# Performance work log

Measured on AMD Instinct MI355X. Metric: run time of the kernel, lower is better.

## Reference

```python
import jax, jax.numpy as jnp
import numpy as np

K = 16

def _knn_idx(pts, k):
    # pts: [B, 3, N] -> idx [B, N, k] (self-inclusive nearest neighbors)
    inner = -2.0 * jnp.einsum('bdn,bdm->bnm', pts, pts)
    xx = jnp.sum(pts * pts, axis=1)  # [B, N]
    pd = -xx[:, :, None] - inner - xx[:, None, :]  # negative squared distance
    _, idx = jax.lax.top_k(pd, k)
    return idx

def _gather(feats, idx):
    # feats: [B, N, D], idx: [B, N, k] -> [B, N, k, D]
    return jax.vmap(lambda f, i: f[i])(feats, idx)

def _conv1x1(x, w, b):
    # x: [B, Cin, N], w: [Cout, Cin], b: [Cout]
    return jnp.einsum('oi,bin->bon', w, x) + b[None, :, None]

def _linear(x, w, b):
    # x: [B, N, Din], w: [Dout, Din]
    return jnp.einsum('bnd,od->bno', x, w) + b

def _local_cov(pts, idx):
    # pts: [B, 3, N] -> [B, 12, N]
    nb = _gather(jnp.swapaxes(pts, 1, 2), idx)  # [B, N, k, 3]
    outer = nb[:, :, 0, :, None] * nb[:, :, 1, None, :]  # [B, N, 3, 3]
    B, N = pts.shape[0], pts.shape[2]
    outer = jnp.swapaxes(outer.reshape(B, N, 9), 1, 2)  # [B, 9, N]
    return jnp.concatenate([pts, outer], axis=1)

def _local_maxpool(x, idx):
    # x: [B, D, N] -> [B, N, D]
    nb = _gather(jnp.swapaxes(x, 1, 2), idx)  # [B, N, k, D]
    return jnp.max(nb, axis=2)

def setup_inputs() -> dict:
    key = jax.random.key(0)
    ks = jax.random.split(key, 20)
    def w(k, shape):
        return jax.random.normal(k, shape, dtype=jnp.float32) * 0.05
    pts = jax.random.normal(ks[0], (8, 3, 4096), dtype=jnp.float32)
    return {
        'pts': pts,
        'm1w1': w(ks[1], (64, 12)), 'm1b1': w(ks[2], (64,)),
        'm1w2': w(ks[3], (64, 64)), 'm1b2': w(ks[4], (64,)),
        'm1w3': w(ks[5], (64, 64)), 'm1b3': w(ks[6], (64,)),
        'l1w': w(ks[7], (64, 64)), 'l1b': w(ks[8], (64,)),
        'c1w': w(ks[9], (128, 64)), 'c1b': w(ks[10], (128,)),
        'l2w': w(ks[11], (128, 128)), 'l2b': w(ks[12], (128,)),
        'c2w': w(ks[13], (1024, 128)), 'c2b': w(ks[14], (1024,)),
        'm2w1': w(ks[15], (512, 1024)), 'm2b1': w(ks[16], (512,)),
        'm2w2': w(ks[17], (512, 512)), 'm2b2': w(ks[18], (512,)),
    }

def reference(pts, m1w1, m1b1, m1w2, m1b2, m1w3, m1b3, l1w, l1b,
              c1w, c1b, l2w, l2b, c2w, c2b, m2w1, m2b1, m2w2, m2b2):
    idx = _knn_idx(pts, K)  # [B, N, k]
    x = _local_cov(pts, idx)  # [B, 12, N]
    # mlp1: three 1x1 convs with ReLU
    x = jax.nn.relu(_conv1x1(x, m1w1, m1b1))
    x = jax.nn.relu(_conv1x1(x, m1w2, m1b2))
    x = jax.nn.relu(_conv1x1(x, m1w3, m1b3))  # [B, 64, N]
    # graph layer
    x = _local_maxpool(x, idx)          # [B, N, 64]
    x = _linear(x, l1w, l1b)            # [B, N, 64]
    x = jnp.swapaxes(x, 1, 2)           # [B, 64, N]
    x = jax.nn.relu(_conv1x1(x, c1w, c1b))  # [B, 128, N]
    x = _local_maxpool(x, idx)          # [B, N, 128]
    x = _linear(x, l2w, l2b)            # [B, N, 128]
    x = jnp.swapaxes(x, 1, 2)           # [B, 128, N]
    x = _conv1x1(x, c2w, c2b)           # [B, 1024, N]
    # global max pool
    x = jnp.max(x, axis=2, keepdims=True)  # [B, 1024, 1]
    # mlp2
    x = jax.nn.relu(_conv1x1(x, m2w1, m2b1))
    x = _conv1x1(x, m2w2, m2b2)  # [B, 512, 1]
    return x.reshape(-1, 512)
```

## Files before the change

### kernel.cpp

```cpp
#include <hip/hip_runtime.h>
#include <cfloat>

#define NBATCH 8
#define NPTS   4096
#define KNN    16
#define PPB    32
#define NSL    8
#define CAP    24

typedef unsigned short u16;
typedef unsigned int   u32;
typedef __attribute__((ext_vector_type(8))) short short8;
typedef __attribute__((ext_vector_type(4))) float f32x4;

__device__ __forceinline__ float relu_f(float x) { return x > 0.f ? x : 0.f; }

__device__ __forceinline__ u32 bf16_split_pack(float v)
{
    unsigned u = __float_as_uint(v);
    unsigned hb = (u + 0x7FFFu + ((u >> 16) & 1u)) >> 16;
    float hf = __uint_as_float(hb << 16);
    float l = v - hf;
    unsigned ul = __float_as_uint(l);
    unsigned lb = (ul + 0x7FFFu + ((ul >> 16) & 1u)) >> 16;
    return (hb << 16) | (lb & 0xFFFFu);
}

__device__ __forceinline__ void unpack8(uint4 a, uint4 b, short8& h, short8& l)
{
    union { unsigned u[4]; short8 s; } H, L;
    H.u[0] = __builtin_amdgcn_perm(a.y, a.x, 0x07060302);
    H.u[1] = __builtin_amdgcn_perm(a.w, a.z, 0x07060302);
    H.u[2] = __builtin_amdgcn_perm(b.y, b.x, 0x07060302);
    H.u[3] = __builtin_amdgcn_perm(b.w, b.z, 0x07060302);
    L.u[0] = __builtin_amdgcn_perm(a.y, a.x, 0x05040100);
    L.u[1] = __builtin_amdgcn_perm(a.w, a.z, 0x05040100);
    L.u[2] = __builtin_amdgcn_perm(b.y, b.x, 0x05040100);
    L.u[3] = __builtin_amdgcn_perm(b.w, b.z, 0x05040100);
    h = H.s; l = L.s;
}

__global__ __launch_bounds__(256)
void knn_kernel(const float* __restrict__ pts, int* __restrict__ idxout)
{
    __shared__ __align__(16) float4 tile[NSL * 129];
    __shared__ float  kl[PPB * NSL * 8];
    __shared__ float  thr[PPB];
    __shared__ int    cnt[PPB];

    const int b = blockIdx.y, tid = threadIdx.x;
    const int ptl = tid >> 3, r = tid & 7;
    const int n = blockIdx.x * PPB + ptl;
    const float* pb = pts + (size_t)b * 3 * NPTS;

    const float sx = pb[n], sy = pb[NPTS + n], sz = pb[2 * NPTS + n];

    float k8[8];
#pragma unroll
    for (int s = 0; s < 8; ++s) k8[s] = -FLT_MAX;

    const float4* slice = tile + r * 129;

    for (int t = 0; t < 4; ++t) {
        if (t) __syncthreads();
        for (int i = tid; i < 1024; i += 256) {
            int j = t * 1024 + i;
            float x = pb[j], y = pb[NPTS + j], z = pb[2 * NPTS + j];
            float xx = __fadd_rn(__fadd_rn(__fmul_rn(x, x), __fmul_rn(y, y)),
                                 __fmul_rn(z, z));
            tile[(i >> 7) * 129 + (i & 127)] = make_float4(x, y, z, xx);
        }
        __syncthreads();
#pragma unroll 8
        for (int ii = 0; ii < 128; ++ii) {
            float4 c = slice[ii];
            float dt = __fmaf_rn(sx, c.x, __fmaf_rn(sy, c.y, __fmul_rn(sz, c.z)));
            float pd = __fmaf_rn(2.f, dt, -c.w);
            float old0 = k8[0];
#pragma unroll
            for (int s = 7; s >= 1; --s)
                k8[s] = __builtin_amdgcn_fmed3f(k8[s - 1], k8[s], pd);
            k8[0] = fmaxf(old0, pd);
        }
    }

#pragma unroll
    for (int s = 0; s < 8; ++s) kl[(ptl * NSL + r) * 8 + s] = k8[s];
    __syncthreads();

    if (r == 0) {
        const float* L = kl + ptl * 64;
        int p0 = 0, p1 = 0, p2 = 0, p3 = 0, p4 = 0, p5 = 0, p6 = 0, p7 = 0;
        float tv = 0.f;
        for (int o = 0; o < 16; ++o) {
            float v0 = (p0 < 8) ? L[p0]      : -FLT_MAX;
            float v1 = (p1 < 8) ? L[8 + p1]  : -FLT_MAX;
            float v2 = (p2 < 8) ? L[16 + p2] : -FLT_MAX;
            float v3 = (p3 < 8) ? L[24 + p3] : -FLT_MAX;
            float v4 = (p4 < 8) ? L[32 + p4] : -FLT_MAX;
            float v5 = (p5 < 8) ? L[40 + p5] : -FLT_MAX;
            float v6 = (p6 < 8) ? L[48 + p6] : -FLT_MAX;
            float v7 = (p7 < 8) ? L[56 + p7] : -FLT_MAX;
            float m = fmaxf(fmaxf(fmaxf(v0, v1), fmaxf(v2, v3)),
                            fmaxf(fmaxf(v4, v5), fmaxf(v6, v7)));
            tv = m;
            if      (v0 == m) ++p0;
            else if (v1 == m) ++p1;
            else if (v2 == m) ++p2;
            else if (v3 == m) ++p3;
            else if (v4 == m) ++p4;
            else if (v5 == m) ++p5;
            else if (v6 == m) ++p6;
            else              ++p7;
        }
        thr[ptl] = tv;
        cnt[ptl] = 0;
    }
    __syncthreads();
    const float myThr = thr[ptl];

    float* pv = kl;
    int*   pi = (int*)(kl + PPB * CAP);

    for (int tt = 0; tt < 4; ++tt) {
        int t = 3 - tt;
        if (tt) {
            __syncthreads();
            for (int i = tid; i < 1024; i += 256) {
                int j = t * 1024 + i;
                float x = pb[j], y = pb[NPTS + j], z = pb[2 * NPTS + j];
                float xx = __fadd_rn(__fadd_rn(__fmul_rn(x, x), __fmul_rn(y, y)),
                                     __fmul_rn(z, z));
                tile[(i >> 7) * 129 + (i & 127)] = make_float4(x, y, z, xx);
            }
            __syncthreads();
        }
#pragma unroll 8
        for (int ii = 0; ii < 128; ++ii) {
            float4 c = slice[ii];
            float dt = __fmaf_rn(sx, c.x, __fmaf_rn(sy, c.y, __fmul_rn(sz, c.z)));
            float pd = __fmaf_rn(2.f, dt, -c.w);
            if (pd >= myThr) {
                int pos = atomicAdd(&cnt[ptl], 1);
                if (pos < CAP) {
                    pv[ptl * CAP + pos] = pd;
                    pi[ptl * CAP + pos] = t * 1024 + r * 128 + ii;
                }
            }
        }
    }
    __syncthreads();

    if (tid < PPB) {
        const int np = blockIdx.x * PPB + tid;
        int* out = idxout + ((size_t)b * NPTS + np) * KNN;
        int c = cnt[tid];
        if (c <= CAP) {
            float* v  = pv + tid * CAP;
            int*   ix = pi + tid * CAP;
            for (int o = 0; o < 16; ++o) {
                int best = o;
                for (int q = o + 1; q < c; ++q) {
                    float vq = v[q], vb = v[best];
                    if (vq > vb || (vq == vb && ix[q] < ix[best])) best = q;
                }
                float tv = v[o]; v[o] = v[best]; v[best] = tv;
                int   ti = ix[o]; ix[o] = ix[best]; ix[best] = ti;
                out[o] = ix[o];
            }
        } else {
            float qx = pb[np], qy = pb[NPTS + np], qz = pb[2 * NPTS + np];
            float v16[16]; int i16[16];
#pragma unroll
            for (int s = 0; s < 16; ++s) { v16[s] = -FLT_MAX; i16[s] = 0; }
            for (int j = 0; j < NPTS; ++j) {
                float x = pb[j], y = pb[NPTS + j], z = pb[2 * NPTS + j];
                float xx = __fadd_rn(__fadd_rn(__fmul_rn(x, x), __fmul_rn(y, y)),
                                     __fmul_rn(z, z));
                float dt = __fmaf_rn(qx, x, __fmaf_rn(qy, y, __fmul_rn(qz, z)));
                float pd = __fmaf_rn(2.f, dt, -xx);
                if (pd > v16[15]) {
                    int s = 15;
                    while (s > 0 && pd > v16[s - 1]) {
                        v16[s] = v16[s - 1]; i16[s] = i16[s - 1]; --s;
                    }
                    v16[s] = pd; i16[s] = j;
                }
            }
            for (int o = 0; o < 16; ++o) out[o] = i16[o];
        }
    }
}

__global__ __launch_bounds__(256)
void cov_mlp1_kernel(const float* __restrict__ pts, const int* __restrict__ idx,
                     const float* __restrict__ w1, const float* __restrict__ b1,
                     const float* __restrict__ w2, const float* __restrict__ b2,
                     const float* __restrict__ w3, const float* __restrict__ b3,
                     float* __restrict__ h3out)
{
    __shared__ __align__(16) float cov[64 * 16];
    __shared__ __align__(16) float w1s[64 * 16];
    __shared__ __align__(16) float w2s[64 * 68];
    __shared__ __align__(16) float w3s[64 * 68];
    __shared__ __align__(16) float hA[64 * 68];
    __shared__ __align__(16) float hB[64 * 68];

    const int b = blockIdx.y, tid = threadIdx.x;
    const int n0 = blockIdx.x * 64;
    const int pq = tid >> 4, cq = tid & 15;

    for (int i = tid; i < 64 * 4; i += 256) {
        int p = i >> 2, k4 = i & 3;
        float4 v = make_float4(0.f, 0.f, 0.f, 0.f);
        if (k4 < 3) v = *(const float4*)(w1 + p * 12 + k4 * 4);
        ((float4*)(w1s + p * 16))[k4] = v;
    }
    for (int i = tid; i < 64 * 16; i += 256) {
        int p = i >> 4, k4 = i & 15;
        ((float4*)(w2s + p * 68))[k4] = ((const float4*)(w2 + p * 64))[k4];
        ((float4*)(w3s + p * 68))[k4] = ((const float4*)(w3 + p * 64))[k4];
    }
    if (tid < 64) {
        const int n = n0 + tid;
        const int* ip = idx + ((size_t)b * NPTS + n) * KNN;
        int j0 = ip[0], j1 = ip[1];
        const float* pb = pts + (size_t)b * 3 * NPTS;
        float px = pb[n],  py = pb[NPTS + n],  pz = pb[2 * NPTS + n];
        float ax = pb[j0], ay = pb[NPTS + j0], az = pb[2 * NPTS + j0];
        float bx = pb[j1], by = pb[NPTS + j1], bz = pb[2 * NPTS + j1];
        float* cv = cov + tid * 16;
        cv[0] = px; cv[1] = py; cv[2] = pz;
        cv[3] = ax * bx; cv[4]  = ax * by; cv[5]  = ax * bz;
        cv[6] = ay * bx; cv[7]  = ay * by; cv[8]  = ay * bz;
        cv[9] = az * bx; cv[10] = az * by; cv[11] = az * bz;
        cv[12] = 0.f; cv[13] = 0.f; cv[14] = 0.f; cv[15] = 0.f;
    }
    __syncthreads();

    {
        float acc[4][4];
#pragma unroll
        for (int i = 0; i < 4; ++i)
#pragma unroll
            for (int j = 0; j < 4; ++j) acc[i][j] = 0.f;
        const float4* X4 = (const float4*)cov;
        const float4* W4 = (const float4*)w1s;
#pragma unroll
        for (int k4 = 0; k4 < 4; ++k4) {
            float4 xa[4], wb[4];
#pragma unroll
            for (int i = 0; i < 4; ++i) xa[i] = X4[(pq * 4 + i) * 4 + k4];
#pragma unroll
            for (int j = 0; j < 4; ++j) wb[j] = W4[(cq + 16 * j) * 4 + k4];
#pragma unroll
            for (int i = 0; i < 4; ++i)
#pragma unroll
                for (int j = 0; j < 4; ++j)
                    acc[i][j] += xa[i].x * wb[j].x + xa[i].y * wb[j].y
                               + xa[i].z * wb[j].z + xa[i].w * wb[j].w;
        }
#pragma unroll
        for (int j = 0; j < 4; ++j) {
            int c = cq + 16 * j;
            float bias = b1[c];
#pragma unroll
            for (int i = 0; i < 4; ++i)
                hA[(pq * 4 + i) * 68 + c] = relu_f(acc[i][j] + bias);
        }
    }
    __syncthreads();

    {
        float acc[4][4];
#pragma unroll
        for (int i = 0; i < 4; ++i)
#pragma unroll
            for (int j = 0; j < 4; ++j) acc[i][j] = 0.f;
        const float4* X4 = (const float4*)hA;
        const float4* W4 = (const float4*)w2s;
        for (int k4 = 0; k4 < 16; ++k4) {
            float4 xa[4], wb[4];
#pragma unroll
            for (int i = 0; i < 4; ++i) xa[i] = X4[(pq * 4 + i) * 17 + k4];
#pragma unroll
            for (int j = 0; j < 4; ++j) wb[j] = W4[(cq + 16 * j) * 17 + k4];
#pragma unroll
            for (int i = 0; i < 4; ++i)
#pragma unroll
                for (int j = 0; j < 4; ++j)
                    acc[i][j] += xa[i].x * wb[j].x + xa[i].y * wb[j].y
                               + xa[i].z * wb[j].z + xa[i].w * wb[j].w;
        }
#pragma unroll
        for (int j = 0; j < 4; ++j) {
            int c = cq + 16 * j;
            float bias = b2[c];
#pragma unroll
            for (int i = 0; i < 4; ++i)
                hB[(pq * 4 + i) * 68 + c] = relu_f(acc[i][j] + bias);
        }
    }
    __syncthreads();

    {
        float acc[4][4];
#pragma unroll
        for (int i = 0; i < 4; ++i)
#pragma unroll
            for (int j = 0; j < 4; ++j) acc[i][j] = 0.f;
        const float4* X4 = (const float4*)hB;
        const float4* W4 = (const float4*)w3s;
        for (int k4 = 0; k4 < 16; ++k4) {
            float4 xa[4], wb[4];
#pragma unroll
            for (int i = 0; i < 4; ++i) xa[i] = X4[(pq * 4 + i) * 17 + k4];
#pragma unroll
            for (int j = 0; j < 4; ++j) wb[j] = W4[(cq + 16 * j) * 17 + k4];
#pragma unroll
            for (int i = 0; i < 4; ++i)
#pragma unroll
                for (int j = 0; j < 4; ++j)
                    acc[i][j] += xa[i].x * wb[j].x + xa[i].y * wb[j].y
                               + xa[i].z * wb[j].z + xa[i].w * wb[j].w;
        }
#pragma unroll
        for (int j = 0; j < 4; ++j) {
            int c = cq + 16 * j;
            float bias = b3[c];
#pragma unroll
            for (int i = 0; i < 4; ++i)
                h3out[((size_t)b * NPTS + n0 + pq * 4 + i) * 64 + c] =
                    relu_f(acc[i][j] + bias);
        }
    }
}

template <int DV4>
__global__ __launch_bounds__(256)
void maxpool4_kernel(const float4* __restrict__ f, const int* __restrict__ idx,
                     float4* __restrict__ out)
{
    constexpr int SH = (DV4 == 16) ? 4 : 5;
    int t = blockIdx.x * 256 + threadIdx.x;
    int d4 = t & (DV4 - 1);
    int n  = (t >> SH) & (NPTS - 1);
    int b  = t >> (SH + 12);
    const int* ip = idx + ((size_t)b * NPTS + n) * KNN;
    const float4* fb = f + (size_t)b * NPTS * DV4;
    float4 v = make_float4(-FLT_MAX, -FLT_MAX, -FLT_MAX, -FLT_MAX);
#pragma unroll
    for (int k = 0; k < KNN; ++k) {
        float4 c = fb[(size_t)ip[k] * DV4 + d4];
        v.x = fmaxf(v.x, c.x); v.y = fmaxf(v.y, c.y);
        v.z = fmaxf(v.z, c.z); v.w = fmaxf(v.w, c.w);
    }
    out[t] = v;
}

__global__ __launch_bounds__(256)
void lin_conv1_kernel(const float* __restrict__ xin,
                      const float* __restrict__ l1w, const float* __restrict__ l1b,
                      const float* __restrict__ c1w, const float* __restrict__ c1b,
                      float* __restrict__ yout)
{
    __shared__ __align__(16) float sx[64 * 68];
    __shared__ __align__(16) float wbuf[64 * 68];
    __shared__ __align__(16) float t1[64 * 68];
    const int b = blockIdx.y, tid = threadIdx.x;
    const int n0 = blockIdx.x * 64;
    const int pq = tid >> 4, cq = tid & 15;

    for (int i = tid; i < 64 * 16; i += 256) {
        int p = i >> 4, k4 = i & 15;
        ((float4*)(sx + p * 68))[k4] =
            ((const float4*)(xin + ((size_t)b * NPTS + n0 + p) * 64))[k4];
        ((float4*)(wbuf + p * 68))[k4] = ((const float4*)(l1w + p * 64))[k4];
    }
    __syncthreads();

    {
        float acc[4][4];
#pragma unroll
        for (int i = 0; i < 4; ++i)
#pragma unroll
            for (int j = 0; j < 4; ++j) acc[i][j] = 0.f;
        const float4* X4 = (const float4*)sx;
        const float4* W4 = (const float4*)wbuf;
        for (int k4 = 0; k4 < 16; ++k4) {
            float4 xa[4], wb[4];
#pragma unroll
            for (int i = 0; i < 4; ++i) xa[i] = X4[(pq * 4 + i) * 17 + k4];
#pragma unroll
            for (int j = 0; j < 4; ++j) wb[j] = W4[(cq + 16 * j) * 17 + k4];
#pragma unroll
            for (int i = 0; i < 4; ++i)
#pragma unroll
                for (int j = 0; j < 4; ++j)
                    acc[i][j] += xa[i].x * wb[j].x + xa[i].y * wb[j].y
                               + xa[i].z * wb[j].z + xa[i].w * wb[j].w;
        }
#pragma unroll
        for (int j = 0; j < 4; ++j) {
            int c = cq + 16 * j;
            float bias = l1b[c];
#pragma unroll
            for (int i = 0; i < 4; ++i)
                t1[(pq * 4 + i) * 68 + c] = acc[i][j] + bias;
        }
    }

    for (int g = 0; g < 2; ++g) {
        __syncthreads();
        for (int i = tid; i < 64 * 16; i += 256) {
            int p = i >> 4, k4 = i & 15;
            ((float4*)(wbuf + p * 68))[k4] =
                ((const float4*)(c1w + (size_t)(g * 64 + p) * 64))[k4];
        }
        __syncthreads();
        float acc[4][4];
#pragma unroll
        for (int i = 0; i < 4; ++i)
#pragma unroll
            for (int j = 0; j < 4; ++j) acc[i][j] = 0.f;
        const float4* X4 = (const float4*)t1;
        const float4* W4 = (const float4*)wbuf;
        for (int k4 = 0; k4 < 16; ++k4) {
            float4 xa[4], wb[4];
#pragma unroll
            for (int i = 0; i < 4; ++i) xa[i] = X4[(pq * 4 + i) * 17 + k4];
#pragma unroll
            for (int j = 0; j < 4; ++j) wb[j] = W4[(cq + 16 * j) * 17 + k4];
#pragma unroll
            for (int i = 0; i < 4; ++i)
#pragma unroll
                for (int j = 0; j < 4; ++j)
                    acc[i][j] += xa[i].x * wb[j].x + xa[i].y * wb[j].y
                               + xa[i].z * wb[j].z + xa[i].w * wb[j].w;
        }
#pragma unroll
        for (int j = 0; j < 4; ++j) {
            int c = g * 64 + cq + 16 * j;
            float bias = c1b[c];
#pragma unroll
            for (int i = 0; i < 4; ++i)
                yout[((size_t)b * NPTS + n0 + pq * 4 + i) * 128 + c] =
                    relu_f(acc[i][j] + bias);
        }
    }
}

__global__ __launch_bounds__(256)
void lin2_kernel(const float* __restrict__ xin, const float* __restrict__ w,
                 const float* __restrict__ bias, u32* __restrict__ xpk)
{
    __shared__ __align__(16) float Xs[64 * 132];
    __shared__ __align__(16) float Ws[64 * 132];
    const int chunk = blockIdx.x, g = blockIdx.y, b = blockIdx.z;
    const int tid = threadIdx.x;

    for (int i = tid; i < 64 * 32; i += 256) {
        int p = i >> 5, k4 = i & 31;
        ((float4*)(Xs + p * 132))[k4] =
            ((const float4*)(xin + ((size_t)b * NPTS + chunk * 64 + p) * 128))[k4];
        ((float4*)(Ws + p * 132))[k4] =
            ((const float4*)(w + (size_t)(g * 64 + p) * 128))[k4];
    }
    __syncthreads();

    const int pq = tid >> 4, cq = tid & 15;
    const float4* X4 = (const float4*)Xs;
    const float4* W4 = (const float4*)Ws;
    float acc[4][4];
#pragma unroll
    for (int i = 0; i < 4; ++i)
#pragma unroll
        for (int j = 0; j < 4; ++j) acc[i][j] = 0.f;

    for (int k4 = 0; k4 < 32; ++k4) {
        float4 xa[4], wb[4];
#pragma unroll
        for (int i = 0; i < 4; ++i) xa[i] = X4[(pq * 4 + i) * 33 + k4];
#pragma unroll
        for (int j = 0; j < 4; ++j) wb[j] = W4[(cq + 16 * j) * 33 + k4];
#pragma unroll
        for (int i = 0; i < 4; ++i)
#pragma unroll
            for (int j = 0; j < 4; ++j)
                acc[i][j] += xa[i].x * wb[j].x + xa[i].y * wb[j].y
                           + xa[i].z * wb[j].z + xa[i].w * wb[j].w;
    }
#pragma unroll
    for (int j = 0; j < 4; ++j) {
        int c = g * 64 + cq + 16 * j;
        float bv = bias[c];
#pragma unroll
        for (int i = 0; i < 4; ++i) {
            float v = acc[i][j] + bv;
            size_t oidx = ((size_t)b * NPTS + chunk * 64 + pq * 4 + i) * 128 + c;
            xpk[oidx] = bf16_split_pack(v);
        }
    }
}

__global__ __launch_bounds__(256)
void wsplit_kernel(const float* __restrict__ w, u32* __restrict__ wpk)
{
    int t = blockIdx.x * 256 + threadIdx.x;
    wpk[t] = bf16_split_pack(w[t]);
}

__global__ __launch_bounds__(256)
void conv2max_mfma(const u32* __restrict__ xpk, const u32* __restrict__ wpk,
                   const float* __restrict__ bias, float* __restrict__ pmax)
{
    __shared__ __align__(16) u16 lds[4 * 16384];
    u16* Wh = lds;
    u16* Wl = lds + 16384;
    u16* Xh = lds + 2 * 16384;
    u16* Xl = lds + 3 * 16384;

    const int chunk = blockIdx.x, g = blockIdx.y, b = blockIdx.z;
    const int tid = threadIdx.x;
    const int lane = tid & 63, wave = tid >> 6;
    const int l15 = lane & 15, l4 = lane >> 4;
    const int wm = wave >> 1, wn = wave & 1;

    const u32* wp_g = wpk + (size_t)g * 128 * 128;
    const u32* xp_g = xpk + ((size_t)b * NPTS + chunk * 128) * 128;

    for (int u = tid; u < 2048; u += 256) {
        int row = u & 127, seg = u >> 7;
        int go = row * 128 + seg * 8;
        int lo_ = seg * 1024 + row * 8;
        uint4 a = *(const uint4*)&wp_g[go];
        uint4 b4 = *(const uint4*)&wp_g[go + 4];
        short8 h, l;
        unpack8(a, b4, h, l);
        *(short8*)&Wh[lo_] = h; *(short8*)&Wl[lo_] = l;
        a = *(const uint4*)&xp_g[go];
        b4 = *(const uint4*)&xp_g[go + 4];
        unpack8(a, b4, h, l);
        *(short8*)&Xh[lo_] = h; *(short8*)&Xl[lo_] = l;
    }
    __syncthreads();

    f32x4 acc[4][4];
#pragma unroll
    for (int mt = 0; mt < 4; ++mt)
#pragma unroll
        for (int nt = 0; nt < 4; ++nt)
            acc[mt][nt] = (f32x4){0.f, 0.f, 0.f, 0.f};

    for (int kb = 0; kb < 4; ++kb) {
        const int seg = kb * 4 + l4;
        short8 Ah[4], Al[4], Bh[4], Bl[4];
#pragma unroll
        for (int mt = 0; mt < 4; ++mt) {
            int off = seg * 1024 + (wm * 64 + mt * 16 + l15) * 8;
            Ah[mt] = *(const short8*)&Wh[off];
            Al[mt] = *(const short8*)&Wl[off];
        }
#pragma unroll
        for (int nt = 0; nt < 4; ++nt) {
            int off = seg * 1024 + (wn * 64 + nt * 16 + l15) * 8;
            Bh[nt] = *(const short8*)&Xh[off];
            Bl[nt] = *(const short8*)&Xl[off];
        }
#pragma unroll
        for (int mt = 0; mt < 4; ++mt)
#pragma unroll
            for (int nt = 0; nt < 4; ++nt) {
                acc[mt][nt] = __builtin_amdgcn_mfma_f32_16x16x32_bf16(
                    Ah[mt], Bh[nt], acc[mt][nt], 0, 0, 0);
                acc[mt][nt] = __builtin_amdgcn_mfma_f32_16x16x32_bf16(
                    Ah[mt], Bl[nt], acc[mt][nt], 0, 0, 0);
                acc[mt][nt] = __builtin_amdgcn_mfma_f32_16x16x32_bf16(
                    Al[mt], Bh[nt], acc[mt][nt], 0, 0, 0);
            }
    }

    __syncthreads();
    float* smax = (float*)lds;
#pragma unroll
    for (int mt = 0; mt < 4; ++mt)
#pragma unroll
        for (int r = 0; r < 4; ++r) {
            float m = fmaxf(fmaxf(acc[mt][0][r], acc[mt][1][r]),
                            fmaxf(acc[mt][2][r], acc[mt][3][r]));
            int c = wm * 64 + mt * 16 + 4 * l4 + r;
            smax[c * 33 + wn * 16 + l15] = m;
        }
    __syncthreads();
    if (tid < 128) {
        const float* row = smax + tid * 33;
        float v = row[0];
#pragma unroll
        for (int j = 1; j < 32; ++j) v = fmaxf(v, row[j]);
        int c = g * 128 + tid;
        pmax[((size_t)b * 32 + chunk) * 1024 + c] = v + bias[c];
    }
}

__global__ __launch_bounds__(256)
void gmax_kernel(const float* __restrict__ pmax, float* __restrict__ gmax)
{
    int t = blockIdx.x * 256 + threadIdx.x;
    int b = t >> 10, ch = t & 1023;
    const float* pp = pmax + (size_t)b * 32 * 1024 + ch;
    float v = -FLT_MAX;
    for (int c = 0; c < 32; ++c) v = fmaxf(v, pp[c * 1024]);
    gmax[t] = v;
}

__global__ __launch_bounds__(128)
void mlp2a_kernel(const float* __restrict__ g, const float* __restrict__ w1,
                  const float* __restrict__ b1, float* __restrict__ h)
{
    __shared__ __align__(16) float sg[1024];
    const int b = blockIdx.y, tid = threadIdx.x;
    for (int i = tid; i < 1024; i += 128) sg[i] = g[b * 1024 + i];
    __syncthreads();
    const int ch = blockIdx.x * 128 + tid;
    const float4* xr = (const float4*)sg;
    const float4* wr = (const float4*)(w1 + (size_t)ch * 1024);
    float a0 = 0.f, a1 = 0.f, a2 = 0.f, a3 = 0.f;
    for (int k = 0; k < 256; ++k) {
        float4 w = wr[k], x = xr[k];
        a0 += w.x * x.x; a1 += w.y * x.y; a2 += w.z * x.z; a3 += w.w * x.w;
    }
    h[b * 512 + ch] = relu_f(b1[ch] + ((a0 + a1) + (a2 + a3)));
}

__global__ __launch_bounds__(128)
void mlp2b_kernel(const float* __restrict__ h, const float* __restrict__ w2,
                  const float* __restrict__ b2, float* __restrict__ out)
{
    __shared__ __align__(16) float sh[512];
    const int b = blockIdx.y, tid = threadIdx.x;
    for (int i = tid; i < 512; i += 128) sh[i] = h[b * 512 + i];
    __syncthreads();
    const int ch = blockIdx.x * 128 + tid;
    const float4* xr = (const float4*)sh;
    const float4* wr = (const float4*)(w2 + (size_t)ch * 512);
    float a0 = 0.f, a1 = 0.f, a2 = 0.f, a3 = 0.f;
    for (int k = 0; k < 128; ++k) {
        float4 w = wr[k], x = xr[k];
        a0 += w.x * x.x; a1 += w.y * x.y; a2 += w.z * x.z; a3 += w.w * x.w;
    }
    out[b * 512 + ch] = b2[ch] + ((a0 + a1) + (a2 + a3));
}

extern "C" void kernel_launch(void* const* d_in, const int* in_sizes, int n_in,
                              void* d_out, int out_size, void* d_ws, size_t ws_size,
                              hipStream_t stream)
{
    const float* pts  = (const float*)d_in[0];
    const float* m1w1 = (const float*)d_in[1];
    const float* m1b1 = (const float*)d_in[2];
    const float* m1w2 = (const float*)d_in[3];
    const float* m1b2 = (const float*)d_in[4];
    const float* m1w3 = (const float*)d_in[5];
    const float* m1b3 = (const float*)d_in[6];
    const float* l1w  = (const float*)d_in[7];
    const float* l1b  = (const float*)d_in[8];
    const float* c1w  = (const float*)d_in[9];
    const float* c1b  = (const float*)d_in[10];
    const float* l2w  = (const float*)d_in[11];
    const float* l2b  = (const float*)d_in[12];
    const float* c2w  = (const float*)d_in[13];
    const float* c2b  = (const float*)d_in[14];
    const float* m2w1 = (const float*)d_in[15];
    const float* m2b1 = (const float*)d_in[16];
    const float* m2w2 = (const float*)d_in[17];
    const float* m2b2 = (const float*)d_in[18];

    char* ws = (char*)d_ws;
    size_t off = 0;
    int*   idx   = (int*)(ws + off);   off += (size_t)NBATCH * NPTS * KNN * 4;
    float* h3    = (float*)(ws + off); off += (size_t)NBATCH * NPTS * 64 * 4;
    float* mp1   = (float*)(ws + off); off += (size_t)NBATCH * NPTS * 64 * 4;
    float* y1    = (float*)(ws + off); off += (size_t)NBATCH * NPTS * 128 * 4;
    float* mp2   = (float*)(ws + off); off += (size_t)NBATCH * NPTS * 128 * 4;
    float* pmaxb = (float*)(ws + off); off += (size_t)NBATCH * 64 * 1024 * 4;
    float* gmx   = (float*)(ws + off); off += (size_t)NBATCH * 1024 * 4;
    float* hbuf  = (float*)(ws + off); off += (size_t)NBATCH * 512 * 4;
    u32*   wpk   = (u32*)(ws + off);   off += (size_t)1024 * 128 * 4;
    u32*   xpk   = (u32*)y1;

    wsplit_kernel<<<dim3(512), 256, 0, stream>>>(c2w, wpk);
    knn_kernel<<<dim3(NPTS / PPB, NBATCH), 256, 0, stream>>>(pts, idx);
    cov_mlp1_kernel<<<dim3(64, NBATCH), 256, 0, stream>>>(pts, idx, m1w1, m1b1,
                                                          m1w2, m1b2, m1w3, m1b3, h3);
    maxpool4_kernel<16><<<dim3(NBATCH * NPTS * 16 / 256), 256, 0, stream>>>(
        (const float4*)h3, idx, (float4*)mp1);
    lin_conv1_kernel<<<dim3(64, NBATCH), 256, 0, stream>>>(mp1, l1w, l1b, c1w, c1b, y1);
    maxpool4_kernel<32><<<dim3(NBATCH * NPTS * 32 / 256), 256, 0, stream>>>(
        (const float4*)y1, idx, (float4*)mp2);
    lin2_kernel<<<dim3(64, 2, NBATCH), 256, 0, stream>>>(mp2, l2w, l2b, xpk);
    conv2max_mfma<<<dim3(32, 8, NBATCH), 256, 0, stream>>>(xpk, wpk, c2b, pmaxb);
    gmax_kernel<<<dim3(32), 256, 0, stream>>>(pmaxb, gmx);
    mlp2a_kernel<<<dim3(4, NBATCH), 128, 0, stream>>>(gmx, m2w1, m2b1, hbuf);
    mlp2b_kernel<<<dim3(4, NBATCH), 128, 0, stream>>>(hbuf, m2w2, m2b2, (float*)d_out);
}
```

Baseline: 299.0 us.

## Split KNN candidate range in halves with two queries per thread, then merge

The KNN kernel now handles 64 query points per block. Each thread keeps two top-8 lists, for queries A and B, so every shared-memory tile load is reused across two queries. Each block scans only half of the candidate points, giving a grid of 64x2x8 blocks, and writes a partial top-16 of values and indices into the y1 scratch buffer. A new merge kernel combines the two sorted halves into the final indices. This adds an extra launch and global traffic for the partial results, plus higher register pressure from the doubled top-k state.

```diff
diff --git a/kernel.cpp b/kernel.cpp
--- a/kernel.cpp
+++ b/kernel.cpp
@@ -4,9 +4,8 @@
 #define NBATCH 8
 #define NPTS   4096
 #define KNN    16
-#define PPB    32
-#define NSL    8
 #define CAP    24
+#define JH     2048
 
 typedef unsigned short u16;
 typedef unsigned int   u32;
@@ -41,55 +40,67 @@
 }
 
 __global__ __launch_bounds__(256)
-void knn_kernel(const float* __restrict__ pts, int* __restrict__ idxout)
-{
-    __shared__ __align__(16) float4 tile[NSL * 129];
-    __shared__ float  kl[PPB * NSL * 8];
-    __shared__ float  thr[PPB];
-    __shared__ int    cnt[PPB];
-
-    const int b = blockIdx.y, tid = threadIdx.x;
+void knn_half_kernel(const float* __restrict__ pts,
+                     float* __restrict__ ppd, int* __restrict__ pix)
+{
+    __shared__ __align__(16) float4 tile[8 * 65];
+    __shared__ float kl[64 * 64];
+    __shared__ float thr[64];
+    __shared__ int   cnt[64];
+
+    const int b = blockIdx.z, half = blockIdx.y, tid = threadIdx.x;
     const int ptl = tid >> 3, r = tid & 7;
-    const int n = blockIdx.x * PPB + ptl;
+    const int n0 = blockIdx.x * 64;
+    const int nA = n0 + ptl, nB = n0 + 32 + ptl;
     const float* pb = pts + (size_t)b * 3 * NPTS;
-
-    const float sx = pb[n], sy = pb[NPTS + n], sz = pb[2 * NPTS + n];
-
-    float k8[8];
-#pragma unroll
-    for (int s = 0; s < 8; ++s) k8[s] = -FLT_MAX;
-
-    const float4* slice = tile + r * 129;
+    const int jb0 = half * JH;
+
+    const float axp = pb[nA], ayp = pb[NPTS + nA], azp = pb[2 * NPTS + nA];
+    const float bxp = pb[nB], byp = pb[NPTS + nB], bzp = pb[2 * NPTS + nB];
+
+    float kA[8], kB[8];
+#pragma unroll
+    for (int s = 0; s < 8; ++s) { kA[s] = -FLT_MAX; kB[s] = -FLT_MAX; }
+
+    const float4* slice = tile + r * 65;
 
     for (int t = 0; t < 4; ++t) {
         if (t) __syncthreads();
-        for (int i = tid; i < 1024; i += 256) {
-            int j = t * 1024 + i;
+        for (int i = tid; i < 512; i += 256) {
+            int j = jb0 + t * 512 + i;
             float x = pb[j], y = pb[NPTS + j], z = pb[2 * NPTS + j];
             float xx = __fadd_rn(__fadd_rn(__fmul_rn(x, x), __fmul_rn(y, y)),
                                  __fmul_rn(z, z));
-            tile[(i >> 7) * 129 + (i & 127)] = make_float4(x, y, z, xx);
+            tile[(i >> 6) * 65 + (i & 63)] = make_float4(x, y, z, xx);
         }
         __syncthreads();
 #pragma unroll 8
-        for (int ii = 0; ii < 128; ++ii) {
+        for (int ii = 0; ii < 64; ++ii) {
             float4 c = slice[ii];
-            float dt = __fmaf_rn(sx, c.x, __fmaf_rn(sy, c.y, __fmul_rn(sz, c.z)));
-            float pd = __fmaf_rn(2.f, dt, -c.w);
-            float old0 = k8[0];
-#pragma unroll
-            for (int s = 7; s >= 1; --s)
-                k8[s] = __builtin_amdgcn_fmed3f(k8[s - 1], k8[s], pd);
-            k8[0] = fmaxf(old0, pd);
-        }
-    }
-
-#pragma unroll
-    for (int s = 0; s < 8; ++s) kl[(ptl * NSL + r) * 8 + s] = k8[s];
-    __syncthreads();
-
-    if (r == 0) {
-        const float* L = kl + ptl * 64;
+            float dA = __fmaf_rn(axp, c.x, __fmaf_rn(ayp, c.y, __fmul_rn(azp, c.z)));
+            float pdA = __fmaf_rn(2.f, dA, -c.w);
+            float dB = __fmaf_rn(bxp, c.x, __fmaf_rn(byp, c.y, __fmul_rn(bzp, c.z)));
+            float pdB = __fmaf_rn(2.f, dB, -c.w);
+            float oA = kA[0], oB = kB[0];
+#pragma unroll
+            for (int s = 7; s >= 1; --s) {
+                kA[s] = __builtin_amdgcn_fmed3f(kA[s - 1], kA[s], pdA);
+                kB[s] = __builtin_amdgcn_fmed3f(kB[s - 1], kB[s], pdB);
+            }
+            kA[0] = fmaxf(oA, pdA);
+            kB[0] = fmaxf(oB, pdB);
+        }
+    }
+
+#pragma unroll
+    for (int s = 0; s < 8; ++s) {
+        kl[ptl * 64 + r * 8 + s] = kA[s];
+        kl[(32 + ptl) * 64 + r * 8 + s] = kB[s];
+    }
+    __syncthreads();
+
+    if (tid < 64) {
+        const float* L = kl + tid * 64;
         int p0 = 0, p1 = 0, p2 = 0, p3 = 0, p4 = 0, p5 = 0, p6 = 0, p7 = 0;
         float tv = 0.f;
         for (int o = 0; o < 16; ++o) {
@@ -113,47 +124,53 @@
             else if (v6 == m) ++p6;
             else              ++p7;
         }
-        thr[ptl] = tv;
-        cnt[ptl] = 0;
-    }
-    __syncthreads();
-    const float myThr = thr[ptl];
+        thr[tid] = tv;
+        cnt[tid] = 0;
+    }
+    __syncthreads();
+    const float thrA = thr[ptl], thrB = thr[32 + ptl];
 
     float* pv = kl;
-    int*   pi = (int*)(kl + PPB * CAP);
+    int*   pi = (int*)(kl + 64 * CAP);
 
     for (int tt = 0; tt < 4; ++tt) {
         int t = 3 - tt;
         if (tt) {
             __syncthreads();
-            for (int i = tid; i < 1024; i += 256) {
-                int j = t * 1024 + i;
+            for (int i = tid; i < 512; i += 256) {
+                int j = jb0 + t * 512 + i;
                 float x = pb[j], y = pb[NPTS + j], z = pb[2 * NPTS + j];
                 float xx = __fadd_rn(__fadd_rn(__fmul_rn(x, x), __fmul_rn(y, y)),
                                      __fmul_rn(z, z));
-                tile[(i >> 7) * 129 + (i & 127)] = make_float4(x, y, z, xx);
+                tile[(i >> 6) * 65 + (i & 63)] = make_float4(x, y, z, xx);
             }
             __syncthreads();
         }
 #pragma unroll 8
-        for (int ii = 0; ii < 128; ++ii) {
+        for (int ii = 0; ii < 64; ++ii) {
             float4 c = slice[ii];
-            float dt = __fmaf_rn(sx, c.x, __fmaf_rn(sy, c.y, __fmul_rn(sz, c.z)));
-            float pd = __fmaf_rn(2.f, dt, -c.w);
-            if (pd >= myThr) {
+            float dA = __fmaf_rn(axp, c.x, __fmaf_rn(ayp, c.y, __fmul_rn(azp, c.z)));
+            float pdA = __fmaf_rn(2.f, dA, -c.w);
+            float dB = __fmaf_rn(bxp, c.x, __fmaf_rn(byp, c.y, __fmul_rn(bzp, c.z)));
+            float pdB = __fmaf_rn(2.f, dB, -c.w);
+            int j = jb0 + t * 512 + r * 64 + ii;
+            if (pdA >= thrA) {
                 int pos = atomicAdd(&cnt[ptl], 1);
-                if (pos < CAP) {
-                    pv[ptl * CAP + pos] = pd;
-                    pi[ptl * CAP + pos] = t * 1024 + r * 128 + ii;
-                }
+                if (pos < CAP) { pv[ptl * CAP + pos] = pdA; pi[ptl * CAP + pos] = j; }
             }
-        }
-    }
-    __syncthreads();
-
-    if (tid < PPB) {
-        const int np = blockIdx.x * PPB + tid;
-        int* out = idxout + ((size_t)b * NPTS + np) * KNN;
+            if (pdB >= thrB) {
+                int pos = atomicAdd(&cnt[32 + ptl], 1);
+                if (pos < CAP) { pv[(32 + ptl) * CAP + pos] = pdB;
+                                 pi[(32 + ptl) * CAP + pos] = j; }
+            }
+        }
+    }
+    __syncthreads();
+
+    if (tid < 64) {
+        const int np = n0 + tid;
+        float* od = ppd + (((size_t)b * 2 + half) * NPTS + np) * KNN;
+        int*   oi = pix + (((size_t)b * 2 + half) * NPTS + np) * KNN;
         int c = cnt[tid];
         if (c <= CAP) {
             float* v  = pv + tid * CAP;
@@ -166,14 +183,14 @@
                 }
                 float tv = v[o]; v[o] = v[best]; v[best] = tv;
                 int   ti = ix[o]; ix[o] = ix[best]; ix[best] = ti;
-                out[o] = ix[o];
+                od[o] = v[o]; oi[o] = ix[o];
             }
         } else {
             float qx = pb[np], qy = pb[NPTS + np], qz = pb[2 * NPTS + np];
             float v16[16]; int i16[16];
 #pragma unroll
             for (int s = 0; s < 16; ++s) { v16[s] = -FLT_MAX; i16[s] = 0; }
-            for (int j = 0; j < NPTS; ++j) {
+            for (int j = jb0; j < jb0 + JH; ++j) {
                 float x = pb[j], y = pb[NPTS + j], z = pb[2 * NPTS + j];
                 float xx = __fadd_rn(__fadd_rn(__fmul_rn(x, x), __fmul_rn(y, y)),
                                      __fmul_rn(z, z));
@@ -187,8 +204,29 @@
                     v16[s] = pd; i16[s] = j;
                 }
             }
-            for (int o = 0; o < 16; ++o) out[o] = i16[o];
-        }
+            for (int o = 0; o < 16; ++o) { od[o] = v16[o]; oi[o] = i16[o]; }
+        }
+    }
+}
+
+__global__ __launch_bounds__(256)
+void knn_merge_kernel(const float* __restrict__ ppd, const int* __restrict__ pix,
+                      int* __restrict__ idxout)
+{
+    int t = blockIdx.x * 256 + threadIdx.x;
+    int b = t >> 12, n = t & 4095;
+    const float* A  = ppd + (((size_t)b * 2 + 0) * NPTS + n) * KNN;
+    const int*   Ai = pix + (((size_t)b * 2 + 0) * NPTS + n) * KNN;
+    const float* B  = ppd + (((size_t)b * 2 + 1) * NPTS + n) * KNN;
+    const int*   Bi = pix + (((size_t)b * 2 + 1) * NPTS + n) * KNN;
+    int* out = idxout + ((size_t)b * NPTS + n) * KNN;
+    int ia = 0, ib = 0;
+#pragma unroll
+    for (int o = 0; o < 16; ++o) {
+        float va = A[ia], vb = B[ib];
+        bool takeA = (va > vb) || (va == vb && Ai[ia] < Bi[ib]);
+        out[o] = takeA ? Ai[ia] : Bi[ib];
+        ia += takeA; ib += !takeA;
     }
 }
 
@@ -687,9 +725,12 @@
     float* hbuf  = (float*)(ws + off); off += (size_t)NBATCH * 512 * 4;
     u32*   wpk   = (u32*)(ws + off);   off += (size_t)1024 * 128 * 4;
     u32*   xpk   = (u32*)y1;
+    float* ppd   = (float*)y1;
+    int*   pix   = (int*)((char*)y1 + (size_t)NBATCH * 2 * NPTS * KNN * 4);
 
     wsplit_kernel<<<dim3(512), 256, 0, stream>>>(c2w, wpk);
-    knn_kernel<<<dim3(NPTS / PPB, NBATCH), 256, 0, stream>>>(pts, idx);
+    knn_half_kernel<<<dim3(64, 2, NBATCH), 256, 0, stream>>>(pts, ppd, pix);
+    knn_merge_kernel<<<dim3(128), 256, 0, stream>>>(ppd, pix, idx);
     cov_mlp1_kernel<<<dim3(64, NBATCH), 256, 0, stream>>>(pts, idx, m1w1, m1b1,
                                                           m1w2, m1b2, m1w3, m1b3, h3);
     maxpool4_kernel<16><<<dim3(NBATCH * NPTS * 16 / 256), 256, 0, stream>>>(
```

After: 308.4 us. 3.1% more time.

## Split KNN candidate scan into two halves and merge partial top-k lists

Applied to the files above, without the earlier changes.

The KNN kernel now scans half of the candidate points per block, doubling the grid from 1024 to 2048 blocks, and writes a sorted partial top-16 (distances and indices) per half into scratch space reused from the y1 buffer. A new merge kernel combines the two sorted lists per query point, breaking ties by lower index. This aims to raise occupancy and parallelism on the dominant KNN stage and shorten each block's serial scan. The cost is an extra kernel launch, extra global traffic for the partial results, and duplicated threshold work per half.

```diff
diff --git a/kernel.cpp b/kernel.cpp
--- a/kernel.cpp
+++ b/kernel.cpp
@@ -7,6 +7,7 @@
 #define PPB    32
 #define NSL    8
 #define CAP    24
+#define JH     2048
 
 typedef unsigned short u16;
 typedef unsigned int   u32;
@@ -41,17 +42,19 @@
 }
 
 __global__ __launch_bounds__(256)
-void knn_kernel(const float* __restrict__ pts, int* __restrict__ idxout)
+void knn_half_kernel(const float* __restrict__ pts,
+                     float* __restrict__ ppd, int* __restrict__ pix)
 {
     __shared__ __align__(16) float4 tile[NSL * 129];
     __shared__ float  kl[PPB * NSL * 8];
     __shared__ float  thr[PPB];
     __shared__ int    cnt[PPB];
 
-    const int b = blockIdx.y, tid = threadIdx.x;
+    const int b = blockIdx.z, half = blockIdx.y, tid = threadIdx.x;
     const int ptl = tid >> 3, r = tid & 7;
     const int n = blockIdx.x * PPB + ptl;
     const float* pb = pts + (size_t)b * 3 * NPTS;
+    const int jb0 = half * JH;
 
     const float sx = pb[n], sy = pb[NPTS + n], sz = pb[2 * NPTS + n];
 
@@ -61,10 +64,10 @@
 
     const float4* slice = tile + r * 129;
 
-    for (int t = 0; t < 4; ++t) {
+    for (int t = 0; t < 2; ++t) {
         if (t) __syncthreads();
         for (int i = tid; i < 1024; i += 256) {
-            int j = t * 1024 + i;
+            int j = jb0 + t * 1024 + i;
             float x = pb[j], y = pb[NPTS + j], z = pb[2 * NPTS + j];
             float xx = __fadd_rn(__fadd_rn(__fmul_rn(x, x), __fmul_rn(y, y)),
                                  __fmul_rn(z, z));
@@ -122,12 +125,12 @@
     float* pv = kl;
     int*   pi = (int*)(kl + PPB * CAP);
 
-    for (int tt = 0; tt < 4; ++tt) {
-        int t = 3 - tt;
+    for (int tt = 0; tt < 2; ++tt) {
+        int t = 1 - tt;
         if (tt) {
             __syncthreads();
             for (int i = tid; i < 1024; i += 256) {
-                int j = t * 1024 + i;
+                int j = jb0 + t * 1024 + i;
                 float x = pb[j], y = pb[NPTS + j], z = pb[2 * NPTS + j];
                 float xx = __fadd_rn(__fadd_rn(__fmul_rn(x, x), __fmul_rn(y, y)),
                                      __fmul_rn(z, z));
@@ -144,7 +147,7 @@
                 int pos = atomicAdd(&cnt[ptl], 1);
                 if (pos < CAP) {
                     pv[ptl * CAP + pos] = pd;
-                    pi[ptl * CAP + pos] = t * 1024 + r * 128 + ii;
+                    pi[ptl * CAP + pos] = jb0 + t * 1024 + r * 128 + ii;
                 }
             }
         }
@@ -153,7 +156,8 @@
 
     if (tid < PPB) {
         const int np = blockIdx.x * PPB + tid;
-        int* out = idxout + ((size_t)b * NPTS + np) * KNN;
+        float* od = ppd + (((size_t)b * 2 + half) * NPTS + np) * KNN;
+        int*   oi = pix + (((size_t)b * 2 + half) * NPTS + np) * KNN;
         int c = cnt[tid];
         if (c <= CAP) {
             float* v  = pv + tid * CAP;
@@ -166,14 +170,14 @@
                 }
                 float tv = v[o]; v[o] = v[best]; v[best] = tv;
                 int   ti = ix[o]; ix[o] = ix[best]; ix[best] = ti;
-                out[o] = ix[o];
+                od[o] = v[o]; oi[o] = ix[o];
             }
         } else {
             float qx = pb[np], qy = pb[NPTS + np], qz = pb[2 * NPTS + np];
             float v16[16]; int i16[16];
 #pragma unroll
             for (int s = 0; s < 16; ++s) { v16[s] = -FLT_MAX; i16[s] = 0; }
-            for (int j = 0; j < NPTS; ++j) {
+            for (int j = jb0; j < jb0 + JH; ++j) {
                 float x = pb[j], y = pb[NPTS + j], z = pb[2 * NPTS + j];
                 float xx = __fadd_rn(__fadd_rn(__fmul_rn(x, x), __fmul_rn(y, y)),
                                      __fmul_rn(z, z));
@@ -187,8 +191,29 @@
                     v16[s] = pd; i16[s] = j;
                 }
             }
-            for (int o = 0; o < 16; ++o) out[o] = i16[o];
-        }
+            for (int o = 0; o < 16; ++o) { od[o] = v16[o]; oi[o] = i16[o]; }
+        }
+    }
+}
+
+__global__ __launch_bounds__(256)
+void knn_merge_kernel(const float* __restrict__ ppd, const int* __restrict__ pix,
+                      int* __restrict__ idxout)
+{
+    int t = blockIdx.x * 256 + threadIdx.x;
+    int b = t >> 12, n = t & 4095;
+    const float* A  = ppd + (((size_t)b * 2 + 0) * NPTS + n) * KNN;
+    const int*   Ai = pix + (((size_t)b * 2 + 0) * NPTS + n) * KNN;
+    const float* B  = ppd + (((size_t)b * 2 + 1) * NPTS + n) * KNN;
+    const int*   Bi = pix + (((size_t)b * 2 + 1) * NPTS + n) * KNN;
+    int* out = idxout + ((size_t)b * NPTS + n) * KNN;
+    int ia = 0, ib = 0;
+#pragma unroll
+    for (int o = 0; o < 16; ++o) {
+        float va = A[ia], vb = B[ib];
+        bool takeA = (va > vb) || (va == vb && Ai[ia] < Bi[ib]);
+        out[o] = takeA ? Ai[ia] : Bi[ib];
+        ia += takeA; ib += !takeA;
     }
 }
 
@@ -687,9 +712,12 @@
     float* hbuf  = (float*)(ws + off); off += (size_t)NBATCH * 512 * 4;
     u32*   wpk   = (u32*)(ws + off);   off += (size_t)1024 * 128 * 4;
     u32*   xpk   = (u32*)y1;
+    float* ppd   = (float*)y1;
+    int*   pix   = (int*)((char*)y1 + (size_t)NBATCH * 2 * NPTS * KNN * 4);
 
     wsplit_kernel<<<dim3(512), 256, 0, stream>>>(c2w, wpk);
-    knn_kernel<<<dim3(NPTS / PPB, NBATCH), 256, 0, stream>>>(pts, idx);
+    knn_half_kernel<<<dim3(NPTS / PPB, 2, NBATCH), 256, 0, stream>>>(pts, ppd, pix);
+    knn_merge_kernel<<<dim3(128), 256, 0, stream>>>(ppd, pix, idx);
     cov_mlp1_kernel<<<dim3(64, NBATCH), 256, 0, stream>>>(pts, idx, m1w1, m1b1,
                                                           m1w2, m1b2, m1w3, m1b3, h3);
     maxpool4_kernel<16><<<dim3(NBATCH * NPTS * 16 / 256), 256, 0, stream>>>(
```

Result: slower. 326.6 us (+9.2%).

## Fuse second local maxpool into lin2 and compute lin2 with split-bf16 MFMA

Applied to the files above, without the earlier changes.

The separate 128-channel neighbor maxpool and the FP32 SIMT lin2 GEMM are replaced by one kernel. It gathers neighbor maxima straight into LDS as split bf16 hi/lo and runs the 128x128 linear on MFMA with three-term split precision. This removes the mp2 intermediate round trip through global memory and one launch, and moves the GEMM onto matrix cores. The grid shrinks to 64x8 blocks, which may limit occupancy for the gather-heavy phase, and l2w needs an extra pre-split launch.

```diff
diff --git a/kernel.cpp b/kernel.cpp
--- a/kernel.cpp
+++ b/kernel.cpp
@@ -451,54 +451,113 @@
 }
 
 __global__ __launch_bounds__(256)
-void lin2_kernel(const float* __restrict__ xin, const float* __restrict__ w,
-                 const float* __restrict__ bias, u32* __restrict__ xpk)
-{
-    __shared__ __align__(16) float Xs[64 * 132];
-    __shared__ __align__(16) float Ws[64 * 132];
-    const int chunk = blockIdx.x, g = blockIdx.y, b = blockIdx.z;
+void mp2lin2_mfma(const float* __restrict__ y1, const int* __restrict__ idx,
+                  const u32* __restrict__ w2pk, const float* __restrict__ bias,
+                  u32* __restrict__ xpk)
+{
+    __shared__ __align__(16) u16 Xh[8 * 64 * 8];
+    __shared__ __align__(16) u16 Xl[8 * 64 * 8];
+    __shared__ __align__(16) u16 Wh[8 * 128 * 8];
+    __shared__ __align__(16) u16 Wl[8 * 128 * 8];
+
+    const int chunk = blockIdx.x, b = blockIdx.y;
     const int tid = threadIdx.x;
-
-    for (int i = tid; i < 64 * 32; i += 256) {
-        int p = i >> 5, k4 = i & 31;
-        ((float4*)(Xs + p * 132))[k4] =
-            ((const float4*)(xin + ((size_t)b * NPTS + chunk * 64 + p) * 128))[k4];
-        ((float4*)(Ws + p * 132))[k4] =
-            ((const float4*)(w + (size_t)(g * 64 + p) * 128))[k4];
-    }
-    __syncthreads();
-
-    const int pq = tid >> 4, cq = tid & 15;
-    const float4* X4 = (const float4*)Xs;
-    const float4* W4 = (const float4*)Ws;
-    float acc[4][4];
-#pragma unroll
-    for (int i = 0; i < 4; ++i)
-#pragma unroll
-        for (int j = 0; j < 4; ++j) acc[i][j] = 0.f;
-
-    for (int k4 = 0; k4 < 32; ++k4) {
-        float4 xa[4], wb[4];
-#pragma unroll
-        for (int i = 0; i < 4; ++i) xa[i] = X4[(pq * 4 + i) * 33 + k4];
-#pragma unroll
-        for (int j = 0; j < 4; ++j) wb[j] = W4[(cq + 16 * j) * 33 + k4];
-#pragma unroll
-        for (int i = 0; i < 4; ++i)
-#pragma unroll
-            for (int j = 0; j < 4; ++j)
-                acc[i][j] += xa[i].x * wb[j].x + xa[i].y * wb[j].y
-                           + xa[i].z * wb[j].z + xa[i].w * wb[j].w;
-    }
-#pragma unroll
-    for (int j = 0; j < 4; ++j) {
-        int c = g * 64 + cq + 16 * j;
-        float bv = bias[c];
-#pragma unroll
-        for (int i = 0; i < 4; ++i) {
-            float v = acc[i][j] + bv;
-            size_t oidx = ((size_t)b * NPTS + chunk * 64 + pq * 4 + i) * 128 + c;
-            xpk[oidx] = bf16_split_pack(v);
+    const int lane = tid & 63, wave = tid >> 6;
+    const int l15 = lane & 15, l4 = lane >> 4;
+    const int wm = wave >> 1, wn = wave & 1;
+
+    f32x4 acc[4][2];
+#pragma unroll
+    for (int mt = 0; mt < 4; ++mt)
+#pragma unroll
+        for (int nt = 0; nt < 2; ++nt)
+            acc[mt][nt] = (f32x4){0.f, 0.f, 0.f, 0.f};
+
+    const int f4 = tid & 15;
+
+    for (int h = 0; h < 2; ++h) {
+        __syncthreads();
+
+        for (int u = tid; u < 1024; u += 256) {
+            int row = u & 127, seg = u >> 7;
+            int go = row * 128 + h * 64 + seg * 8;
+            uint4 a = *(const uint4*)&w2pk[go];
+            uint4 b4 = *(const uint4*)&w2pk[go + 4];
+            short8 hh, ll;
+            unpack8(a, b4, hh, ll);
+            int lo_ = (seg * 128 + row) * 8;
+            *(short8*)&Wh[lo_] = hh; *(short8*)&Wl[lo_] = ll;
+        }
+
+        for (int pass = 0; pass < 4; ++pass) {
+            int ptl = pass * 16 + (tid >> 4);
+            int ptg = chunk * 64 + ptl;
+            const int* ip = idx + ((size_t)b * NPTS + ptg) * KNN;
+            float4 mx = make_float4(-FLT_MAX, -FLT_MAX, -FLT_MAX, -FLT_MAX);
+#pragma unroll
+            for (int k = 0; k < KNN; ++k) {
+                const float4* src = (const float4*)
+                    (y1 + ((size_t)b * NPTS + ip[k]) * 128 + h * 64);
+                float4 c = src[f4];
+                mx.x = fmaxf(mx.x, c.x); mx.y = fmaxf(mx.y, c.y);
+                mx.z = fmaxf(mx.z, c.z); mx.w = fmaxf(mx.w, c.w);
+            }
+            u32 p0 = bf16_split_pack(mx.x), p1 = bf16_split_pack(mx.y);
+            u32 p2 = bf16_split_pack(mx.z), p3 = bf16_split_pack(mx.w);
+            int seg = f4 >> 1, eb = (f4 & 1) * 4;
+            int base = (seg * 64 + ptl) * 8 + eb;
+            uint2 hv, lv;
+            hv.x = (p0 >> 16) | (p1 & 0xFFFF0000u);
+            hv.y = (p2 >> 16) | (p3 & 0xFFFF0000u);
+            lv.x = (p0 & 0xFFFFu) | (p1 << 16);
+            lv.y = (p2 & 0xFFFFu) | (p3 << 16);
+            *(uint2*)&Xh[base] = hv;
+            *(uint2*)&Xl[base] = lv;
+        }
+        __syncthreads();
+
+        for (int kbl = 0; kbl < 2; ++kbl) {
+            const int seg = kbl * 4 + l4;
+            short8 Ah[4], Al[4], Bh[2], Bl[2];
+#pragma unroll
+            for (int mt = 0; mt < 4; ++mt) {
+                int off = (seg * 128 + wm * 64 + mt * 16 + l15) * 8;
+                Ah[mt] = *(const short8*)&Wh[off];
+                Al[mt] = *(const short8*)&Wl[off];
+            }
+#pragma unroll
+            for (int nt = 0; nt < 2; ++nt) {
+                int off = (seg * 64 + wn * 32 + nt * 16 + l15) * 8;
+                Bh[nt] = *(const short8*)&Xh[off];
+                Bl[nt] = *(const short8*)&Xl[off];
+            }
+#pragma unroll
+            for (int mt = 0; mt < 4; ++mt)
+#pragma unroll
+                for (int nt = 0; nt < 2; ++nt) {
+                    acc[mt][nt] = __builtin_amdgcn_mfma_f32_16x16x32_bf16(
+                        Ah[mt], Bh[nt], acc[mt][nt], 0, 0, 0);
+                    acc[mt][nt] = __builtin_amdgcn_mfma_f32_16x16x32_bf16(
+                        Ah[mt], Bl[nt], acc[mt][nt], 0, 0, 0);
+                    acc[mt][nt] = __builtin_amdgcn_mfma_f32_16x16x32_bf16(
+                        Al[mt], Bh[nt], acc[mt][nt], 0, 0, 0);
+                }
+        }
+    }
+
+#pragma unroll
+    for (int mt = 0; mt < 4; ++mt) {
+        int ch = wm * 64 + mt * 16 + 4 * l4;
+        float4 bv = *(const float4*)(bias + ch);
+#pragma unroll
+        for (int nt = 0; nt < 2; ++nt) {
+            int ptg = chunk * 64 + wn * 32 + nt * 16 + l15;
+            uint4 o;
+            o.x = bf16_split_pack(acc[mt][nt][0] + bv.x);
+            o.y = bf16_split_pack(acc[mt][nt][1] + bv.y);
+            o.z = bf16_split_pack(acc[mt][nt][2] + bv.z);
+            o.w = bf16_split_pack(acc[mt][nt][3] + bv.w);
+            *(uint4*)&xpk[((size_t)b * NPTS + ptg) * 128 + ch] = o;
         }
     }
 }
@@ -681,23 +740,22 @@
     float* h3    = (float*)(ws + off); off += (size_t)NBATCH * NPTS * 64 * 4;
     float* mp1   = (float*)(ws + off); off += (size_t)NBATCH * NPTS * 64 * 4;
     float* y1    = (float*)(ws + off); off += (size_t)NBATCH * NPTS * 128 * 4;
-    float* mp2   = (float*)(ws + off); off += (size_t)NBATCH * NPTS * 128 * 4;
+    u32*   xpk   = (u32*)(ws + off);   off += (size_t)NBATCH * NPTS * 128 * 4;
     float* pmaxb = (float*)(ws + off); off += (size_t)NBATCH * 64 * 1024 * 4;
     float* gmx   = (float*)(ws + off); off += (size_t)NBATCH * 1024 * 4;
     float* hbuf  = (float*)(ws + off); off += (size_t)NBATCH * 512 * 4;
     u32*   wpk   = (u32*)(ws + off);   off += (size_t)1024 * 128 * 4;
-    u32*   xpk   = (u32*)y1;
+    u32*   w2pk  = (u32*)(ws + off);   off += (size_t)128 * 128 * 4;
 
     wsplit_kernel<<<dim3(512), 256, 0, stream>>>(c2w, wpk);
+    wsplit_kernel<<<dim3(64), 256, 0, stream>>>(l2w, w2pk);
     knn_kernel<<<dim3(NPTS / PPB, NBATCH), 256, 0, stream>>>(pts, idx);
     cov_mlp1_kernel<<<dim3(64, NBATCH), 256, 0, stream>>>(pts, idx, m1w1, m1b1,
                                                           m1w2, m1b2, m1w3, m1b3, h3);
     maxpool4_kernel<16><<<dim3(NBATCH * NPTS * 16 / 256), 256, 0, stream>>>(
         (const float4*)h3, idx, (float4*)mp1);
     lin_conv1_kernel<<<dim3(64, NBATCH), 256, 0, stream>>>(mp1, l1w, l1b, c1w, c1b, y1);
-    maxpool4_kernel<32><<<dim3(NBATCH * NPTS * 32 / 256), 256, 0, stream>>>(
-        (const float4*)y1, idx, (float4*)mp2);
-    lin2_kernel<<<dim3(64, 2, NBATCH), 256, 0, stream>>>(mp2, l2w, l2b, xpk);
+    mp2lin2_mfma<<<dim3(64, NBATCH), 256, 0, stream>>>(y1, idx, w2pk, l2b, xpk);
     conv2max_mfma<<<dim3(32, 8, NBATCH), 256, 0, stream>>>(xpk, wpk, c2b, pmaxb);
     gmax_kernel<<<dim3(32), 256, 0, stream>>>(pmaxb, gmx);
     mlp2a_kernel<<<dim3(4, NBATCH), 128, 0, stream>>>(gmx, m2w1, m2b1, hbuf);
```

After: 286.9 us. 1.04x faster.
